# Kernel optimization log

Measured on AMD Instinct MI355X. Metric: run time of the kernel, lower is better.

Reference implementation:

```python
import jax, jax.numpy as jnp
import numpy as np

E = 1024  # embedding_dim
H = 64    # head_size

def setup_inputs() -> dict:
    key = jax.random.key(0)
    k1, k2, k3, k4 = jax.random.split(key, 4)
    x = jax.random.normal(k1, (4, 4096, E), dtype=jnp.float32)
    # nn.Linear(E, H, bias=False) weights have shape [H, E]; y = x @ W.T
    s = 1.0 / np.sqrt(E)
    Wq = jax.random.normal(k2, (H, E), dtype=jnp.float32) * s
    Wk = jax.random.normal(k3, (H, E), dtype=jnp.float32) * s
    Wv = jax.random.normal(k4, (H, E), dtype=jnp.float32) * s
    return {"x": x, "Wq": Wq, "Wk": Wk, "Wv": Wv}

def reference(x, Wq, Wk, Wv):
    B, T, E_ = x.shape
    q = jnp.einsum('bte,he->bth', x, Wq)
    k = jnp.einsum('bte,he->bth', x, Wk)
    v = jnp.einsum('bte,he->bth', x, Wv)
    # NOTE: original scales by sqrt(embedding_dim), not head_size
    scores = jnp.einsum('bqh,bkh->bqk', q, k) / jnp.sqrt(jnp.asarray(E_, x.dtype))
    causal = jnp.tril(jnp.ones((T, T), dtype=bool))
    scores = jnp.where(causal, scores, -jnp.inf)
    weights = jax.nn.softmax(scores, axis=-1)
    return jnp.einsum('bqk,bkh->bqh', weights, v)
```

## Files before the change

### kernel.cpp

```cpp
#include <hip/hip_runtime.h>
#include <stdint.h>

typedef __bf16 bf16x8 __attribute__((ext_vector_type(8)));
typedef float  f32x4  __attribute__((ext_vector_type(4)));

#define E_DIM 1024
#define H_DIM 64
#define T_SEQ 4096
#define B_BAT 4
#define M_TOT (B_BAT * T_SEQ)
#define NSPLIT 4

__device__ __forceinline__ ushort f2bfu(float f) {
    return __builtin_bit_cast(ushort, (__bf16)f);
}
__device__ __forceinline__ uint32_t pk2(float lo, float hi) {
    return (uint32_t)f2bfu(lo) | ((uint32_t)f2bfu(hi) << 16);
}
__device__ __forceinline__ float ex2(float x) {
    return __builtin_amdgcn_exp2f(x);
}
__device__ __forceinline__ bf16x8 ldfrag(const ushort* p) {
    return __builtin_bit_cast(bf16x8, *(const uint4*)(p));
}
__device__ __forceinline__ void barrier_lgkm() {
    __builtin_amdgcn_s_waitcnt(0xC07F);
    __builtin_amdgcn_s_barrier();
}

__global__ __launch_bounds__(256) void wcvt(const float* __restrict__ Wq,
                                            const float* __restrict__ Wk,
                                            const float* __restrict__ Wv,
                                            ushort* __restrict__ Wfm) {
    int g = blockIdx.x * 256 + threadIdx.x;
    int n = g >> 7;
    int k8 = g & 127;
    const float* src = (n < 64) ? (Wq + (size_t)n * E_DIM)
                     : (n < 128) ? (Wk + (size_t)(n - 64) * E_DIM)
                     : (Wv + (size_t)(n - 128) * E_DIM);
    float sc = (n < 64) ? 0.045084220f : 1.0f;
    float4 a = *(const float4*)(src + k8 * 8);
    float4 b = *(const float4*)(src + k8 * 8 + 4);
    uint4 o;
    o.x = pk2(a.x * sc, a.y * sc); o.y = pk2(a.z * sc, a.w * sc);
    o.z = pk2(b.x * sc, b.y * sc); o.w = pk2(b.z * sc, b.w * sc);
    int s = k8 >> 3, kc = (k8 >> 2) & 1, qd = k8 & 3;
    int nt = n >> 4, lm = n & 15;
    int lane = qd * 16 + lm;
    *(uint4*)(Wfm + (((size_t)(s * 12 + nt) * 2 + kc) * 64 + lane) * 8) = o;
}

__global__ __launch_bounds__(256, 3) void qkv(const float* __restrict__ x,
                                              const ushort* __restrict__ Wfm,
                                              ushort* __restrict__ Qfm,
                                              ushort* __restrict__ Kfm,
                                              ushort* __restrict__ Vfm) {
    __shared__ union {
        ushort a[2][32 * 72];
        struct { ushort c[32 * 136]; ushort vt[64 * 40]; } epi;
    } sm;
    const int tid = threadIdx.x;
    const int w = tid >> 6, l = tid & 63;
    const int lm = l & 15, qd = l >> 4;
    const int m0 = blockIdx.x * 32;

    f32x4 acc[2][3];
#pragma unroll
    for (int r2 = 0; r2 < 2; ++r2)
#pragma unroll
        for (int t = 0; t < 3; ++t) acc[r2][t] = (f32x4){0.f, 0.f, 0.f, 0.f};

    const int srow = tid >> 3, kseg = tid & 7;
    const float* xsrc = x + (size_t)(m0 + srow) * E_DIM + kseg * 8;

    {
        float4 a0 = *(const float4*)xsrc;
        float4 a1 = *(const float4*)(xsrc + 4);
        uint4 u = {pk2(a0.x, a0.y), pk2(a0.z, a0.w), pk2(a1.x, a1.y), pk2(a1.z, a1.w)};
        *(uint4*)(&sm.a[0][srow * 72 + kseg * 8]) = u;
    }
    float4 xa0 = *(const float4*)(xsrc + 64);
    float4 xa1 = *(const float4*)(xsrc + 68);
    float4 xb0 = *(const float4*)(xsrc + 128);
    float4 xb1 = *(const float4*)(xsrc + 132);
    __syncthreads();

    for (int s = 0; s < 16; ++s) {
        const int cb = s & 1, nb = cb ^ 1;
        float4 xc0 = xa0, xc1 = xa1;
        if (s < 13) {
            xc0 = *(const float4*)(xsrc + (s + 3) * 64);
            xc1 = *(const float4*)(xsrc + (s + 3) * 64 + 4);
        }
        bf16x8 wf[3][2];
#pragma unroll
        for (int t = 0; t < 3; ++t)
#pragma unroll
            for (int kc = 0; kc < 2; ++kc)
                wf[t][kc] = ldfrag(Wfm + (((size_t)(s * 12 + w * 3 + t) * 2 + kc) * 64 + l) * 8);
        bf16x8 af[2][2];
#pragma unroll
        for (int r2 = 0; r2 < 2; ++r2)
#pragma unroll
            for (int kc = 0; kc < 2; ++kc)
                af[r2][kc] = ldfrag(&sm.a[cb][(r2 * 16 + lm) * 72 + kc * 32 + qd * 8]);
#pragma unroll
        for (int t = 0; t < 3; ++t)
#pragma unroll
            for (int kc = 0; kc < 2; ++kc)
#pragma unroll
                for (int r2 = 0; r2 < 2; ++r2)
                    acc[r2][t] = __builtin_amdgcn_mfma_f32_16x16x32_bf16(af[r2][kc], wf[t][kc], acc[r2][t], 0, 0, 0);
        if (s < 15) {
            uint4 u = {pk2(xa0.x, xa0.y), pk2(xa0.z, xa0.w), pk2(xa1.x, xa1.y), pk2(xa1.z, xa1.w)};
            *(uint4*)(&sm.a[nb][srow * 72 + kseg * 8]) = u;
        }
        xa0 = xb0; xa1 = xb1; xb0 = xc0; xb1 = xc1;
        if (s < 15) barrier_lgkm();
    }
    __syncthreads();

#pragma unroll
    for (int r2 = 0; r2 < 2; ++r2)
#pragma unroll
        for (int t = 0; t < 3; ++t) {
            int gc = w * 48 + t * 16 + lm;
            int m = r2 * 16 + qd * 4;
#pragma unroll
            for (int rr = 0; rr < 4; ++rr) {
                ushort v = f2bfu(acc[r2][t][rr]);
                if (gc < 128) sm.epi.c[(m + rr) * 136 + gc] = v;
                else          sm.epi.vt[(gc - 128) * 40 + (m + rr)] = v;
            }
        }
    __syncthreads();

    const int g16b = m0 >> 4;
    const int kt64 = m0 >> 6;
    const int tb   = (m0 >> 4) & 3;
    const int kcv  = (m0 >> 5) & 1;
#pragma unroll
    for (int ii = 0; ii < 3; ++ii) {
        int i = w + ii * 4;
        uint4 val;
        ushort* dst;
        if (i < 4) {
            int qt_l = i >> 1, kc = i & 1;
            val = *(const uint4*)(&sm.epi.c[(qt_l * 16 + lm) * 136 + kc * 32 + qd * 8]);
            dst = Qfm + (((size_t)(g16b + qt_l) * 2 + kc) * 64 + l) * 8;
        } else if (i < 8) {
            int j2 = i - 4, t_l = j2 >> 1, kc = j2 & 1;
            val = *(const uint4*)(&sm.epi.c[(t_l * 16 + lm) * 136 + 64 + kc * 32 + qd * 8]);
            dst = Kfm + (((size_t)((kt64 * 4 + tb + t_l) * 2 + kc)) * 64 + l) * 8;
        } else {
            int t = i - 8;
            val = *(const uint4*)(&sm.epi.vt[(t * 16 + lm) * 40 + qd * 8]);
            dst = Vfm + (((size_t)((kt64 * 4 + t) * 2 + kcv)) * 64 + l) * 8;
        }
        *(uint4*)dst = val;
    }
}

__global__ __launch_bounds__(256, 4) void flash(const ushort* __restrict__ Qfm,
                                                const ushort* __restrict__ Kfm,
                                                const ushort* __restrict__ Vfm,
                                                float* __restrict__ Opart,
                                                float* __restrict__ lpart) {
    __shared__ ushort plds[4][16 * 72];
    const int tid = threadIdx.x;
    const int wv = tid >> 6, l = tid & 63;
    const int lm = l & 15, qd = l >> 4;
    const int pr = blockIdx.x;
    const int bt = blockIdx.y;
    const int h  = blockIdx.z;
    ushort* myp = plds[wv];

#pragma unroll 1
    for (int half = 0; half < 2; ++half) {
        const int qt = half ? (63 - pr) : pr;
        const size_t rowg = (size_t)bt * T_SEQ + qt * 64 + wv * 16;
        const int g16 = bt * 256 + qt * 4 + wv;

        bf16x8 qf0, qf1;
        {
            const ushort* qp = Qfm + ((size_t)g16 * 2) * 512 + l * 8;
            qf0 = ldfrag(qp);
            qf1 = ldfrag(qp + 512);
        }
        f32x4 o[4];
#pragma unroll
        for (int t = 0; t < 4; ++t) o[t] = (f32x4){0.f, 0.f, 0.f, 0.f};
        float lacc = 0.f;

#pragma unroll 1
        for (int kt = h; kt <= qt; kt += NSPLIT) {
            const ushort* kb = Kfm + ((size_t)(bt * 64 + kt) * 8) * 512;
            const ushort* vb = Vfm + ((size_t)(bt * 64 + kt) * 8) * 512;
            f32x4 sf[4];
#pragma unroll
            for (int t = 0; t < 4; ++t) sf[t] = (f32x4){0.f, 0.f, 0.f, 0.f};
#pragma unroll
            for (int t = 0; t < 4; ++t) {
                bf16x8 k0 = ldfrag(kb + (t * 2 + 0) * 512 + l * 8);
                bf16x8 k1 = ldfrag(kb + (t * 2 + 1) * 512 + l * 8);
                sf[t] = __builtin_amdgcn_mfma_f32_16x16x32_bf16(k0, qf0, sf[t], 0, 0, 0);
                sf[t] = __builtin_amdgcn_mfma_f32_16x16x32_bf16(k1, qf1, sf[t], 0, 0, 0);
            }
            uint4 vu[4][2];
#pragma unroll
            for (int t = 0; t < 4; ++t) {
                vu[t][0] = *(const uint4*)(vb + (t * 2 + 0) * 512 + l * 8);
                vu[t][1] = *(const uint4*)(vb + (t * 2 + 1) * 512 + l * 8);
            }
            ushort* wp = myp + lm * 72 + qd * 4;
            if (kt != qt) {
#pragma unroll
                for (int t = 0; t < 4; ++t) {
                    float p0 = ex2(sf[t][0]), p1 = ex2(sf[t][1]);
                    float p2 = ex2(sf[t][2]), p3 = ex2(sf[t][3]);
                    lacc += (p0 + p1) + (p2 + p3);
                    *(uint2*)(wp + t * 16) = uint2{pk2(p0, p1), pk2(p2, p3)};
                }
            } else {
#pragma unroll
                for (int t = 0; t < 4; ++t) {
                    if (t < wv) {
                        float p0 = ex2(sf[t][0]), p1 = ex2(sf[t][1]);
                        float p2 = ex2(sf[t][2]), p3 = ex2(sf[t][3]);
                        lacc += (p0 + p1) + (p2 + p3);
                        *(uint2*)(wp + t * 16) = uint2{pk2(p0, p1), pk2(p2, p3)};
                    } else if (t == wv) {
                        float p[4];
#pragma unroll
                        for (int rr = 0; rr < 4; ++rr) {
                            float pe = ex2(sf[t][rr]);
                            if (qd * 4 + rr > lm) pe = 0.f;
                            lacc += pe;
                            p[rr] = pe;
                        }
                        *(uint2*)(wp + t * 16) = uint2{pk2(p[0], p[1]), pk2(p[2], p[3])};
                    } else {
                        *(uint2*)(wp + t * 16) = uint2{0u, 0u};
                    }
                }
            }
            __builtin_amdgcn_wave_barrier();
            __builtin_amdgcn_s_waitcnt(0xC07F);
            __builtin_amdgcn_wave_barrier();
            bf16x8 pf0 = ldfrag(myp + lm * 72 + qd * 8);
            bf16x8 pf1 = ldfrag(myp + lm * 72 + 32 + qd * 8);
#pragma unroll
            for (int t = 0; t < 4; ++t) {
                bf16x8 v0 = __builtin_bit_cast(bf16x8, vu[t][0]);
                bf16x8 v1 = __builtin_bit_cast(bf16x8, vu[t][1]);
                o[t] = __builtin_amdgcn_mfma_f32_16x16x32_bf16(pf0, v0, o[t], 0, 0, 0);
                o[t] = __builtin_amdgcn_mfma_f32_16x16x32_bf16(pf1, v1, o[t], 0, 0, 0);
            }
            __builtin_amdgcn_wave_barrier();
        }
        lacc += __shfl_xor(lacc, 16);
        lacc += __shfl_xor(lacc, 32);

        float* ob = Opart + ((size_t)h * M_TOT + rowg) * 64;
#pragma unroll
        for (int t = 0; t < 4; ++t)
#pragma unroll
            for (int rr = 0; rr < 4; ++rr)
                ob[(size_t)(qd * 4 + rr) * 64 + t * 16 + lm] = o[t][rr];
        if (qd == 0) lpart[(size_t)h * M_TOT + rowg + lm] = lacc;
    }
}

__global__ __launch_bounds__(256) void combine(const float* __restrict__ Opart,
                                               const float* __restrict__ lpart,
                                               float* __restrict__ out) {
    int i4 = blockIdx.x * 256 + threadIdx.x;
    size_t base = (size_t)i4 * 4;
    int row = i4 >> 4;
    float ls = 0.f;
#pragma unroll
    for (int s = 0; s < NSPLIT; ++s) ls += lpart[(size_t)s * M_TOT + row];
    const size_t SP = (size_t)M_TOT * 64;
    float4 o = {0.f, 0.f, 0.f, 0.f};
#pragma unroll
    for (int s = 0; s < NSPLIT; ++s) {
        float4 a = *(const float4*)(Opart + (size_t)s * SP + base);
        o.x += a.x; o.y += a.y; o.z += a.z; o.w += a.w;
    }
    float inv = 1.0f / ls;
    o.x *= inv; o.y *= inv; o.z *= inv; o.w *= inv;
    *(float4*)(out + base) = o;
}

extern "C" void kernel_launch(void* const* d_in, const int* in_sizes, int n_in,
                              void* d_out, int out_size, void* d_ws, size_t ws_size,
                              hipStream_t stream) {
    const float* x  = (const float*)d_in[0];
    const float* Wq = (const float*)d_in[1];
    const float* Wk = (const float*)d_in[2];
    const float* Wv = (const float*)d_in[3];
    float* out = (float*)d_out;

    char* ws = (char*)d_ws;
    ushort* Wfm = (ushort*)(ws);
    ushort* Qfm = (ushort*)(ws + 393216);
    ushort* Kfm = (ushort*)(ws + 2490368);
    ushort* Vfm = (ushort*)(ws + 4587520);
    float*  Op  = (float*) (ws + 6684672);
    float*  lp  = (float*) (ws + 23461888);

    wcvt<<<96, 256, 0, stream>>>(Wq, Wk, Wv, Wfm);
    qkv<<<512, 256, 0, stream>>>(x, Wfm, Qfm, Kfm, Vfm);
    flash<<<dim3(32, B_BAT, NSPLIT), 256, 0, stream>>>(Qfm, Kfm, Vfm, Op, lp);
    combine<<<1024, 256, 0, stream>>>(Op, lp, out);
}
```

Measured before the change: 135.2 us.

## Split KV range across waves within block and combine partials in LDS

Instead of splitting the key range across four grid blocks and reducing partial outputs in a separate combine kernel, each block now handles one 16-row query group, and its four waves take interleaved key tiles. The per-wave partial outputs and row sums are reduced through shared memory and written straight to the output. This drops the combine kernel launch and the global round trip of partial O and l buffers. In exchange it adds a block-wide sync per query group and extra LDS, and each block now does less work per launch.

```diff
diff --git a/kernel.cpp b/kernel.cpp
--- a/kernel.cpp
+++ b/kernel.cpp
@@ -9,7 +9,6 @@
 #define T_SEQ 4096
 #define B_BAT 4
 #define M_TOT (B_BAT * T_SEQ)
-#define NSPLIT 4
 
 __device__ __forceinline__ ushort f2bfu(float f) {
     return __builtin_bit_cast(ushort, (__bf16)f);
@@ -161,25 +160,26 @@
     }
 }
 
-__global__ __launch_bounds__(256, 4) void flash(const ushort* __restrict__ Qfm,
-                                                const ushort* __restrict__ Kfm,
-                                                const ushort* __restrict__ Vfm,
-                                                float* __restrict__ Opart,
-                                                float* __restrict__ lpart) {
+__global__ __launch_bounds__(256, 4) void flashc(const ushort* __restrict__ Qfm,
+                                                 const ushort* __restrict__ Kfm,
+                                                 const ushort* __restrict__ Vfm,
+                                                 float* __restrict__ out) {
     __shared__ ushort plds[4][16 * 72];
+    __shared__ float  ro[4][16][68];
+    __shared__ float  rl[4][16];
     const int tid = threadIdx.x;
     const int wv = tid >> 6, l = tid & 63;
     const int lm = l & 15, qd = l >> 4;
     const int pr = blockIdx.x;
     const int bt = blockIdx.y;
-    const int h  = blockIdx.z;
     ushort* myp = plds[wv];
 
 #pragma unroll 1
     for (int half = 0; half < 2; ++half) {
-        const int qt = half ? (63 - pr) : pr;
-        const size_t rowg = (size_t)bt * T_SEQ + qt * 64 + wv * 16;
-        const int g16 = bt * 256 + qt * 4 + wv;
+        const int j   = half ? (255 - pr) : pr;
+        const int ktd = j >> 2;
+        const int td  = j & 3;
+        const int g16 = bt * 256 + j;
 
         bf16x8 qf0, qf1;
         {
@@ -193,7 +193,7 @@
         float lacc = 0.f;
 
 #pragma unroll 1
-        for (int kt = h; kt <= qt; kt += NSPLIT) {
+        for (int kt = wv; kt <= ktd; kt += 4) {
             const ushort* kb = Kfm + ((size_t)(bt * 64 + kt) * 8) * 512;
             const ushort* vb = Vfm + ((size_t)(bt * 64 + kt) * 8) * 512;
             f32x4 sf[4];
@@ -213,7 +213,7 @@
                 vu[t][1] = *(const uint4*)(vb + (t * 2 + 1) * 512 + l * 8);
             }
             ushort* wp = myp + lm * 72 + qd * 4;
-            if (kt != qt) {
+            if (kt != ktd) {
 #pragma unroll
                 for (int t = 0; t < 4; ++t) {
                     float p0 = ex2(sf[t][0]), p1 = ex2(sf[t][1]);
@@ -224,12 +224,12 @@
             } else {
 #pragma unroll
                 for (int t = 0; t < 4; ++t) {
-                    if (t < wv) {
+                    if (t < td) {
                         float p0 = ex2(sf[t][0]), p1 = ex2(sf[t][1]);
                         float p2 = ex2(sf[t][2]), p3 = ex2(sf[t][3]);
                         lacc += (p0 + p1) + (p2 + p3);
                         *(uint2*)(wp + t * 16) = uint2{pk2(p0, p1), pk2(p2, p3)};
-                    } else if (t == wv) {
+                    } else if (t == td) {
                         float p[4];
 #pragma unroll
                         for (int rr = 0; rr < 4; ++rr) {
@@ -260,36 +260,30 @@
         }
         lacc += __shfl_xor(lacc, 16);
         lacc += __shfl_xor(lacc, 32);
-
-        float* ob = Opart + ((size_t)h * M_TOT + rowg) * 64;
+        if (qd == 0) rl[wv][lm] = lacc;
 #pragma unroll
         for (int t = 0; t < 4; ++t)
 #pragma unroll
             for (int rr = 0; rr < 4; ++rr)
-                ob[(size_t)(qd * 4 + rr) * 64 + t * 16 + lm] = o[t][rr];
-        if (qd == 0) lpart[(size_t)h * M_TOT + rowg + lm] = lacc;
+                ro[wv][qd * 4 + rr][t * 16 + lm] = o[t][rr];
+        __syncthreads();
+        {
+            const int row = wv * 4 + qd;
+            float ls = rl[0][row] + rl[1][row] + rl[2][row] + rl[3][row];
+            float inv = 1.0f / ls;
+            float4 s0 = *(const float4*)&ro[0][row][lm * 4];
+            float4 s1 = *(const float4*)&ro[1][row][lm * 4];
+            float4 s2 = *(const float4*)&ro[2][row][lm * 4];
+            float4 s3 = *(const float4*)&ro[3][row][lm * 4];
+            float4 ov;
+            ov.x = (s0.x + s1.x + s2.x + s3.x) * inv;
+            ov.y = (s0.y + s1.y + s2.y + s3.y) * inv;
+            ov.z = (s0.z + s1.z + s2.z + s3.z) * inv;
+            ov.w = (s0.w + s1.w + s2.w + s3.w) * inv;
+            *(float4*)(out + ((size_t)bt * T_SEQ + j * 16 + row) * 64 + lm * 4) = ov;
+        }
+        __syncthreads();
     }
-}
-
-__global__ __launch_bounds__(256) void combine(const float* __restrict__ Opart,
-                                               const float* __restrict__ lpart,
-                                               float* __restrict__ out) {
-    int i4 = blockIdx.x * 256 + threadIdx.x;
-    size_t base = (size_t)i4 * 4;
-    int row = i4 >> 4;
-    float ls = 0.f;
-#pragma unroll
-    for (int s = 0; s < NSPLIT; ++s) ls += lpart[(size_t)s * M_TOT + row];
-    const size_t SP = (size_t)M_TOT * 64;
-    float4 o = {0.f, 0.f, 0.f, 0.f};
-#pragma unroll
-    for (int s = 0; s < NSPLIT; ++s) {
-        float4 a = *(const float4*)(Opart + (size_t)s * SP + base);
-        o.x += a.x; o.y += a.y; o.z += a.z; o.w += a.w;
-    }
-    float inv = 1.0f / ls;
-    o.x *= inv; o.y *= inv; o.z *= inv; o.w *= inv;
-    *(float4*)(out + base) = o;
 }
 
 extern "C" void kernel_launch(void* const* d_in, const int* in_sizes, int n_in,
@@ -306,11 +300,8 @@
     ushort* Qfm = (ushort*)(ws + 393216);
     ushort* Kfm = (ushort*)(ws + 2490368);
     ushort* Vfm = (ushort*)(ws + 4587520);
-    float*  Op  = (float*) (ws + 6684672);
-    float*  lp  = (float*) (ws + 23461888);
 
     wcvt<<<96, 256, 0, stream>>>(Wq, Wk, Wv, Wfm);
     qkv<<<512, 256, 0, stream>>>(x, Wfm, Qfm, Kfm, Vfm);
-    flash<<<dim3(32, B_BAT, NSPLIT), 256, 0, stream>>>(Qfm, Kfm, Vfm, Op, lp);
-    combine<<<1024, 256, 0, stream>>>(Op, lp, out);
-}
+    flashc<<<dim3(128, B_BAT), 256, 0, stream>>>(Qfm, Kfm, Vfm, out);
+}
```

Result: no change. 133.4 us (-1.3%).
